# Optimization experiments

Hardware: AMD Instinct MI355X
Metric: run time of the kernel (lower is better)

The kernel has to match this reference:

```python
import jax, jax.numpy as jnp
import numpy as np

N = 100000
E = 1600000
IN_C = 512
HID = 128
OUT_C = 40
NUM_LAYERS = 3
SIGMA = 1.0


def setup_inputs() -> dict:
    key = jax.random.key(0)
    ks = jax.random.split(key, 8)
    x = jax.random.normal(ks[0], (N, IN_C), dtype=jnp.float32)
    edge_index = jax.random.randint(ks[1], (2, E), 0, N, dtype=jnp.int64)
    # input Linear (default torch init scale ~ kaiming uniform; any values fine for a reference)
    W0 = jax.random.normal(ks[2], (HID, IN_C), dtype=jnp.float32) / np.sqrt(IN_C)
    b0 = jnp.zeros((HID,), dtype=jnp.float32)
    # GCNConv weights: normal(0, sigma/sqrt(hidden)) per reset_parameters
    Wc = jax.random.normal(ks[3], (NUM_LAYERS, HID, HID), dtype=jnp.float32) * (SIGMA / np.sqrt(HID))
    bc = jnp.zeros((NUM_LAYERS, HID), dtype=jnp.float32)
    # output Linear
    Wl = jax.random.normal(ks[4], (OUT_C, HID), dtype=jnp.float32) / np.sqrt(HID)
    bl = jnp.zeros((OUT_C,), dtype=jnp.float32)
    return {"x": x, "edge_index": edge_index, "W0": W0, "b0": b0,
            "Wc": Wc, "bc": bc, "Wl": Wl, "bl": bl}


def _gcn_norm(edge_index, num_nodes):
    # PyG GCNConv default: add self-loops, symmetric normalization
    loop = jnp.arange(num_nodes, dtype=edge_index.dtype)
    src = jnp.concatenate([edge_index[0], loop])  # [E + N]
    dst = jnp.concatenate([edge_index[1], loop])
    deg = jax.ops.segment_sum(jnp.ones_like(dst, dtype=jnp.float32), dst,
                              num_segments=num_nodes)
    dinv = jax.lax.rsqrt(deg)  # deg >= 1 thanks to self-loops
    norm = dinv[src] * dinv[dst]  # [E + N]
    return src, dst, norm


def _gcn_conv(h, src, dst, norm, W, b, num_nodes):
    h = h @ W.T                       # [N, HID] transform first (HID small)
    msg = h[src] * norm[:, None]      # gather + scale: [E+N, HID]
    agg = jax.ops.segment_sum(msg, dst, num_segments=num_nodes)
    return agg + b


def reference(x, edge_index, W0, b0, Wc, bc, Wl, bl):
    num_nodes = x.shape[0]
    src, dst, norm = _gcn_norm(edge_index, num_nodes)
    h = jax.nn.relu(x @ W0.T + b0)
    for i in range(Wc.shape[0]):
        h = jax.nn.relu(_gcn_conv(h, src, dst, norm, Wc[i], bc[i], num_nodes))
    logits = h @ Wl.T + bl
    return logits
```

## Files before the change

kernel.cpp:

```cpp
#include <hip/hip_runtime.h>

#define HID 128
#define BSHIFT 10
#define BCAP 20480

typedef _Float16 half8 __attribute__((ext_vector_type(8)));
typedef _Float16 half4v __attribute__((ext_vector_type(4)));
typedef float f32x4 __attribute__((ext_vector_type(4)));


__global__ __launch_bounds__(256) void zero_i32(int* __restrict__ p, int n) {
  int i = blockIdx.x * 256 + threadIdx.x;
  if (i < n) p[i] = 0;
}

__global__ __launch_bounds__(256) void bin_edges(const int* __restrict__ ei,
                                                 int* __restrict__ gcur,
                                                 int2* __restrict__ buf,
                                                 int E, int NB) {
  __shared__ int bcnt[128];
  __shared__ int bbase[128];
  const int tid = threadIdx.x;

  for (int chunk = blockIdx.x * 2048; chunk < E; chunk += gridDim.x * 2048) {
    if (tid < NB) bcnt[tid] = 0;
    __syncthreads();
    int s[8], d[8], slot[8], b[8];
#pragma unroll
    for (int j = 0; j < 8; ++j) {
      int e = chunk + tid + j * 256;
      if (e < E) {
        s[j] = ei[e];
        d[j] = ei[E + e];
        b[j] = d[j] >> BSHIFT;
        slot[j] = atomicAdd(&bcnt[b[j]], 1);
      } else {
        b[j] = -1;
      }
    }
    __syncthreads();
    if (tid < NB && bcnt[tid] > 0) bbase[tid] = atomicAdd(&gcur[tid], bcnt[tid]);
    __syncthreads();
#pragma unroll
    for (int j = 0; j < 8; ++j) {
      if (b[j] >= 0) {
        int pos = bbase[b[j]] + slot[j];
        if (pos < BCAP) buf[(size_t)b[j] * BCAP + pos] = make_int2(s[j], d[j]);
      }
    }
    __syncthreads();
  }
}

__global__ __launch_bounds__(256) void scatter_pad(const int2* __restrict__ buf,
                                                   const int* __restrict__ gcur,
                                                   int* __restrict__ colpad,
                                                   int* __restrict__ cnt,
                                                   float* __restrict__ dinv, int N) {
  __shared__ int lcnt[1 << BSHIFT];
  const int b = blockIdx.x;
  const int base = b << BSHIFT;
  const int tid = threadIdx.x;
  for (int i = tid; i < (1 << BSHIFT); i += 256) lcnt[i] = 0;
  __syncthreads();

  int ne = gcur[b];
  if (ne > BCAP) ne = BCAP;
  const int2* __restrict__ bb = buf + (size_t)b * BCAP;
  for (int i = tid; i < ne; i += 256) {
    int2 p = bb[i];
    int pos = atomicAdd(&lcnt[p.y - base], 1);
    if (pos < 64) colpad[(size_t)p.y * 64 + pos] = p.x;
  }
  __syncthreads();
  for (int i = tid; i < (1 << BSHIFT); i += 256) {
    int n = base + i;
    if (n < N) {
      int c = lcnt[i];
      cnt[n] = c;
      dinv[n] = rsqrtf((float)(c + 1));
    }
  }
}


__global__ __launch_bounds__(256) void cvt_w2(const float* __restrict__ a, int na,
                                              const float* __restrict__ b, int nb,
                                              _Float16* __restrict__ oa,
                                              _Float16* __restrict__ ob) {
  int i = blockIdx.x * 256 + threadIdx.x;
  if (i < na) oa[i] = (_Float16)a[i];
  else if (i < na + nb) ob[i - na] = (_Float16)b[i - na];
}


template <int K, bool CONVA>
__global__ __launch_bounds__(256) void gemm_mfma(const void* __restrict__ Av,
                                                 const _Float16* __restrict__ Wh,
                                                 const float* __restrict__ bias,
                                                 const float* __restrict__ rowscale,
                                                 _Float16* __restrict__ out,
                                                 int N, int do_relu) {
  __shared__ __align__(16) char As[128 * 64 * 2];
  __shared__ __align__(16) char Bs[128 * 64 * 2];

  const int tid = threadIdx.x;
  const int lane = tid & 63;
  const int wave = tid >> 6;
  const int wr = wave >> 1, wc = wave & 1;
  const int row0 = blockIdx.x * 128;

  const float* Af = (const float*)Av;
  const _Float16* Ah = (const _Float16*)Av;

  f32x4 acc[4][4] = {};

  for (int k0 = 0; k0 < K; k0 += 64) {
#pragma unroll
    for (int i = 0; i < 4; ++i) {
      int chunk = tid + i * 256;
      int r = chunk >> 3;
      int q = chunk & 7;
      int gr = row0 + r;
      if (gr >= N) gr = N - 1;
      int byte = (r << 7) | (((q ^ (r & 7)) << 4));
      if (CONVA) {
        const float* src = Af + (size_t)gr * K + k0 + q * 8;
        float4 f0 = *(const float4*)(src);
        float4 f1 = *(const float4*)(src + 4);
        half8 h;
        h[0] = (_Float16)f0.x; h[1] = (_Float16)f0.y;
        h[2] = (_Float16)f0.z; h[3] = (_Float16)f0.w;
        h[4] = (_Float16)f1.x; h[5] = (_Float16)f1.y;
        h[6] = (_Float16)f1.z; h[7] = (_Float16)f1.w;
        *(half8*)(As + byte) = h;
      } else {
        *(half8*)(As + byte) = *(const half8*)(Ah + (size_t)gr * K + k0 + q * 8);
      }
    }
#pragma unroll
    for (int i = 0; i < 4; ++i) {
      int chunk = tid + i * 256;
      int c = chunk >> 3;
      int q = chunk & 7;
      int byte = (c << 7) | (((q ^ (c & 7)) << 4));
      *(half8*)(Bs + byte) = *(const half8*)(Wh + (size_t)c * K + k0 + q * 8);
    }
    __syncthreads();

#pragma unroll
    for (int ks = 0; ks < 2; ++ks) {
      half8 a[4], b[4];
#pragma unroll
      for (int mi = 0; mi < 4; ++mi) {
        int r = wr * 64 + mi * 16 + (lane & 15);
        int q = ks * 4 + (lane >> 4);
        a[mi] = *(const half8*)(As + ((r << 7) | ((q ^ (r & 7)) << 4)));
      }
#pragma unroll
      for (int ni = 0; ni < 4; ++ni) {
        int c = wc * 64 + ni * 16 + (lane & 15);
        int q = ks * 4 + (lane >> 4);
        b[ni] = *(const half8*)(Bs + ((c << 7) | ((q ^ (c & 7)) << 4)));
      }
#pragma unroll
      for (int mi = 0; mi < 4; ++mi)
#pragma unroll
        for (int ni = 0; ni < 4; ++ni)
          acc[mi][ni] = __builtin_amdgcn_mfma_f32_16x16x32_f16(a[mi], b[ni], acc[mi][ni], 0, 0, 0);
    }
    __syncthreads();
  }

  const int cbase = wc * 64 + (lane & 15);
  const int rsub = (lane >> 4) * 4;
#pragma unroll
  for (int mi = 0; mi < 4; ++mi) {
#pragma unroll
    for (int j = 0; j < 4; ++j) {
      int gr = row0 + wr * 64 + mi * 16 + rsub + j;
      if (gr < N) {
        float rs = rowscale ? rowscale[gr] : 1.0f;
#pragma unroll
        for (int ni = 0; ni < 4; ++ni) {
          int c = cbase + ni * 16;
          float v = acc[mi][ni][j] * rs;
          if (bias) v += bias[c];
          if (do_relu) v = fmaxf(v, 0.f);
          out[(size_t)gr * HID + c] = (_Float16)v;
        }
      }
    }
  }
}


__global__ __launch_bounds__(256) void agg_pad(const _Float16* __restrict__ g,
                                               const int* __restrict__ cnt,
                                               const int* __restrict__ colpad,
                                               const float* __restrict__ dinv,
                                               const float* __restrict__ bias,
                                               _Float16* __restrict__ out, int N) {
  int node = blockIdx.x * 4 + (threadIdx.x >> 6);
  if (node >= N) return;
  const int lane = threadIdx.x & 63;
  const int es = lane >> 4;
  const int ch = lane & 15;
  const int deg = cnt[node];
  const int* __restrict__ row = colpad + (size_t)node * 64;

  float acc[8] = {0.f, 0.f, 0.f, 0.f, 0.f, 0.f, 0.f, 0.f};
  int e0 = 0;
  for (; e0 + 16 <= deg; e0 += 16) {
    int i0 = row[e0 + es];
    int i1 = row[e0 + 4 + es];
    int i2 = row[e0 + 8 + es];
    int i3 = row[e0 + 12 + es];
    half8 v0 = *(const half8*)(g + (size_t)i0 * HID + ch * 8);
    half8 v1 = *(const half8*)(g + (size_t)i1 * HID + ch * 8);
    half8 v2 = *(const half8*)(g + (size_t)i2 * HID + ch * 8);
    half8 v3 = *(const half8*)(g + (size_t)i3 * HID + ch * 8);
#pragma unroll
    for (int j = 0; j < 8; ++j)
      acc[j] += ((float)v0[j] + (float)v1[j]) + ((float)v2[j] + (float)v3[j]);
  }
  for (; e0 + 4 <= deg; e0 += 4) {
    int i0 = row[e0 + es];
    half8 v0 = *(const half8*)(g + (size_t)i0 * HID + ch * 8);
#pragma unroll
    for (int j = 0; j < 8; ++j) acc[j] += (float)v0[j];
  }
  const int rem = deg - e0;
  float selfw = 1.0f;
  if (rem > 0) {
    int i0 = (es < rem) ? row[e0 + es] : node;
    half8 v0 = *(const half8*)(g + (size_t)i0 * HID + ch * 8);
#pragma unroll
    for (int j = 0; j < 8; ++j) acc[j] += (float)v0[j];
    selfw = 1.0f - (float)(4 - rem);
  }

#pragma unroll
  for (int j = 0; j < 8; ++j) {
    acc[j] += __shfl_xor(acc[j], 16, 64);
    acc[j] += __shfl_xor(acc[j], 32, 64);
  }

  if (lane < 16) {
    half8 sv = *(const half8*)(g + (size_t)node * HID + ch * 8);
    const float di = dinv[node];
    half8 o;
#pragma unroll
    for (int j = 0; j < 8; ++j) {
      float v = di * (acc[j] + selfw * (float)sv[j]) + bias[ch * 8 + j];
      o[j] = (_Float16)fmaxf(v, 0.f);
    }
    *(half8*)(out + (size_t)node * HID + ch * 8) = o;
  }
}


__global__ __launch_bounds__(256) void gemm40_mfma(const _Float16* __restrict__ h,
                                                   const float* __restrict__ Wl,
                                                   const float* __restrict__ bl,
                                                   float* __restrict__ out, int N) {
  __shared__ __align__(16) _Float16 wlds[48][136];

  const int tid = threadIdx.x;
  const int lane = tid & 63;
  const int wave = tid >> 6;
  const int row0 = blockIdx.x * 128;

#pragma unroll
  for (int i = 0; i < 6; ++i) {
    int idx4 = tid + i * 256;
    int c = idx4 >> 5;
    int ko = (idx4 & 31) * 4;
    float4 v = make_float4(0.f, 0.f, 0.f, 0.f);
    if (c < 40) v = *(const float4*)(Wl + (size_t)c * HID + ko);
    half4v hv;
    hv[0] = (_Float16)v.x; hv[1] = (_Float16)v.y;
    hv[2] = (_Float16)v.z; hv[3] = (_Float16)v.w;
    *(half4v*)&wlds[c][ko] = hv;
  }
  __syncthreads();

  f32x4 acc[2][3] = {};
  const int arow_in = lane & 15;
  const int kq = lane >> 4;

#pragma unroll
  for (int ks = 0; ks < 4; ++ks) {
    half8 a[2], b[3];
#pragma unroll
    for (int mi = 0; mi < 2; ++mi) {
      int gr = row0 + wave * 32 + mi * 16 + arow_in;
      if (gr >= N) gr = N - 1;
      a[mi] = *(const half8*)(h + (size_t)gr * HID + ks * 32 + kq * 8);
    }
#pragma unroll
    for (int ni = 0; ni < 3; ++ni) {
      int c = ni * 16 + arow_in;
      b[ni] = *(const half8*)&wlds[c][ks * 32 + kq * 8];
    }
#pragma unroll
    for (int mi = 0; mi < 2; ++mi)
#pragma unroll
      for (int ni = 0; ni < 3; ++ni)
        acc[mi][ni] = __builtin_amdgcn_mfma_f32_16x16x32_f16(a[mi], b[ni], acc[mi][ni], 0, 0, 0);
  }

  const int rsub = (lane >> 4) * 4;
#pragma unroll
  for (int ni = 0; ni < 3; ++ni) {
    int col = ni * 16 + (lane & 15);
    if (col >= 40) continue;
    float bv = bl[col];
#pragma unroll
    for (int mi = 0; mi < 2; ++mi) {
#pragma unroll
      for (int j = 0; j < 4; ++j) {
        int gr = row0 + wave * 32 + mi * 16 + rsub + j;
        if (gr < N) out[(size_t)gr * 40 + col] = acc[mi][ni][j] + bv;
      }
    }
  }
}


extern "C" void kernel_launch(void* const* d_in, const int* in_sizes, int n_in,
                              void* d_out, int out_size, void* d_ws, size_t ws_size,
                              hipStream_t stream) {
  const float* x = (const float*)d_in[0];
  const int* ei = (const int*)d_in[1];
  const float* W0 = (const float*)d_in[2];
  const float* b0 = (const float*)d_in[3];
  const float* Wc = (const float*)d_in[4];
  const float* bc = (const float*)d_in[5];
  const float* Wl = (const float*)d_in[6];
  const float* bl = (const float*)d_in[7];
  float* out = (float*)d_out;

  const int N = in_sizes[0] / 512;
  const int E = in_sizes[1] / 2;
  const int NB = (N + (1 << BSHIFT) - 1) >> BSHIFT;

  char* ws = (char*)d_ws;
  size_t off = 0;
  auto alloc = [&](size_t bytes) -> char* {
    char* p = ws + off;
    off += (bytes + 511) & ~(size_t)511;
    return p;
  };
  float* dinv = (float*)alloc((size_t)N * 4);
  int* cnt = (int*)alloc((size_t)N * 4);
  int* gcur = (int*)alloc(128 * 4);
  int* colpad = (int*)alloc((size_t)N * 64 * 4);
  int2* bbuf = (int2*)alloc((size_t)NB * BCAP * 8);
  _Float16* hA = (_Float16*)alloc((size_t)N * HID * 2);
  _Float16* hB = (_Float16*)alloc((size_t)N * HID * 2);
  _Float16* hG = (_Float16*)alloc((size_t)N * HID * 2);
  _Float16* W0h = (_Float16*)alloc((size_t)HID * 512 * 2);
  _Float16* Wch = (_Float16*)alloc((size_t)3 * HID * HID * 2);

  const int nb_g = (N + 127) / 128;

  zero_i32<<<1, 256, 0, stream>>>(gcur, 128);
  bin_edges<<<512, 256, 0, stream>>>(ei, gcur, bbuf, E, NB);
  scatter_pad<<<NB, 256, 0, stream>>>(bbuf, gcur, colpad, cnt, dinv, N);

  const int nw0 = HID * 512, nwc = 3 * HID * HID;
  cvt_w2<<<(nw0 + nwc + 255) / 256, 256, 0, stream>>>(W0, nw0, Wc, nwc, W0h, Wch);

  gemm_mfma<512, true><<<nb_g, 256, 0, stream>>>(x, W0h, b0, nullptr, hA, N, 1);

  _Float16* bufs[2] = {hA, hB};
  int cur = 0;
  for (int l = 0; l < 3; ++l) {
    gemm_mfma<128, false><<<nb_g, 256, 0, stream>>>(bufs[cur], Wch + (size_t)l * HID * HID,
                                                    nullptr, dinv, hG, N, 0);
    agg_pad<<<(N + 3) / 4, 256, 0, stream>>>(hG, cnt, colpad, dinv, bc + (size_t)l * HID,
                                             bufs[1 - cur], N);
    cur = 1 - cur;
  }

  gemm40_mfma<<<nb_g, 256, 0, stream>>>(bufs[cur], Wl, bl, out, N);
}
```

Measured before the change: 395.9 us.

## Prefetch next K-tile into registers in GEMM and pre-convert x to fp16

```diff
diff --git a/kernel.cpp b/kernel.cpp
--- a/kernel.cpp
+++ b/kernel.cpp
@@ -93,9 +93,25 @@
   else if (i < na + nb) ob[i - na] = (_Float16)b[i - na];
 }
 
-
-template <int K, bool CONVA>
-__global__ __launch_bounds__(256) void gemm_mfma(const void* __restrict__ Av,
+__global__ __launch_bounds__(256) void cvt_x(const float* __restrict__ in,
+                                             _Float16* __restrict__ out, int n8) {
+  int stride = gridDim.x * 256;
+  for (int i = blockIdx.x * 256 + threadIdx.x; i < n8; i += stride) {
+    const float* src = in + (size_t)i * 8;
+    float4 f0 = *(const float4*)(src);
+    float4 f1 = *(const float4*)(src + 4);
+    half8 h;
+    h[0] = (_Float16)f0.x; h[1] = (_Float16)f0.y;
+    h[2] = (_Float16)f0.z; h[3] = (_Float16)f0.w;
+    h[4] = (_Float16)f1.x; h[5] = (_Float16)f1.y;
+    h[6] = (_Float16)f1.z; h[7] = (_Float16)f1.w;
+    *(half8*)(out + (size_t)i * 8) = h;
+  }
+}
+
+
+template <int K>
+__global__ __launch_bounds__(256) void gemm_mfma(const _Float16* __restrict__ Ah,
                                                  const _Float16* __restrict__ Wh,
                                                  const float* __restrict__ bias,
                                                  const float* __restrict__ rowscale,
@@ -110,41 +126,42 @@
   const int wr = wave >> 1, wc = wave & 1;
   const int row0 = blockIdx.x * 128;
 
-  const float* Af = (const float*)Av;
-  const _Float16* Ah = (const _Float16*)Av;
+  int stbyte[4];
+  const _Float16* asrc[4];
+  const _Float16* bsrc[4];
+#pragma unroll
+  for (int i = 0; i < 4; ++i) {
+    int chunk = tid + i * 256;
+    int r = chunk >> 3, q = chunk & 7;
+    int gr = row0 + r;
+    if (gr >= N) gr = N - 1;
+    stbyte[i] = (r << 7) | ((q ^ (r & 7)) << 4);
+    asrc[i] = Ah + (size_t)gr * K + q * 8;
+    bsrc[i] = Wh + (size_t)r * K + q * 8;
+  }
+
+  half8 ga[4], gb[4];
+#pragma unroll
+  for (int i = 0; i < 4; ++i) {
+    ga[i] = *(const half8*)(asrc[i]);
+    gb[i] = *(const half8*)(bsrc[i]);
+  }
 
   f32x4 acc[4][4] = {};
 
   for (int k0 = 0; k0 < K; k0 += 64) {
+    __syncthreads();
 #pragma unroll
     for (int i = 0; i < 4; ++i) {
-      int chunk = tid + i * 256;
-      int r = chunk >> 3;
-      int q = chunk & 7;
-      int gr = row0 + r;
-      if (gr >= N) gr = N - 1;
-      int byte = (r << 7) | (((q ^ (r & 7)) << 4));
-      if (CONVA) {
-        const float* src = Af + (size_t)gr * K + k0 + q * 8;
-        float4 f0 = *(const float4*)(src);
-        float4 f1 = *(const float4*)(src + 4);
-        half8 h;
-        h[0] = (_Float16)f0.x; h[1] = (_Float16)f0.y;
-        h[2] = (_Float16)f0.z; h[3] = (_Float16)f0.w;
-        h[4] = (_Float16)f1.x; h[5] = (_Float16)f1.y;
-        h[6] = (_Float16)f1.z; h[7] = (_Float16)f1.w;
-        *(half8*)(As + byte) = h;
-      } else {
-        *(half8*)(As + byte) = *(const half8*)(Ah + (size_t)gr * K + k0 + q * 8);
-      }
-    }
-#pragma unroll
-    for (int i = 0; i < 4; ++i) {
-      int chunk = tid + i * 256;
-      int c = chunk >> 3;
-      int q = chunk & 7;
-      int byte = (c << 7) | (((q ^ (c & 7)) << 4));
-      *(half8*)(Bs + byte) = *(const half8*)(Wh + (size_t)c * K + k0 + q * 8);
+      *(half8*)(As + stbyte[i]) = ga[i];
+      *(half8*)(Bs + stbyte[i]) = gb[i];
+    }
+    if (k0 + 64 < K) {
+#pragma unroll
+      for (int i = 0; i < 4; ++i) {
+        ga[i] = *(const half8*)(asrc[i] + k0 + 64);
+        gb[i] = *(const half8*)(bsrc[i] + k0 + 64);
+      }
     }
     __syncthreads();
 
@@ -169,7 +186,6 @@
         for (int ni = 0; ni < 4; ++ni)
           acc[mi][ni] = __builtin_amdgcn_mfma_f32_16x16x32_f16(a[mi], b[ni], acc[mi][ni], 0, 0, 0);
     }
-    __syncthreads();
   }
 
   const int cbase = wc * 64 + (lane & 15);
@@ -357,6 +373,7 @@
   int* gcur = (int*)alloc(128 * 4);
   int* colpad = (int*)alloc((size_t)N * 64 * 4);
   int2* bbuf = (int2*)alloc((size_t)NB * BCAP * 8);
+  _Float16* xh = (_Float16*)alloc((size_t)N * 512 * 2);
   _Float16* hA = (_Float16*)alloc((size_t)N * HID * 2);
   _Float16* hB = (_Float16*)alloc((size_t)N * HID * 2);
   _Float16* hG = (_Float16*)alloc((size_t)N * HID * 2);
@@ -371,14 +388,15 @@
 
   const int nw0 = HID * 512, nwc = 3 * HID * HID;
   cvt_w2<<<(nw0 + nwc + 255) / 256, 256, 0, stream>>>(W0, nw0, Wc, nwc, W0h, Wch);
-
-  gemm_mfma<512, true><<<nb_g, 256, 0, stream>>>(x, W0h, b0, nullptr, hA, N, 1);
+  cvt_x<<<2048, 256, 0, stream>>>(x, xh, N * 64);
+
+  gemm_mfma<512><<<nb_g, 256, 0, stream>>>(xh, W0h, b0, nullptr, hA, N, 1);
 
   _Float16* bufs[2] = {hA, hB};
   int cur = 0;
   for (int l = 0; l < 3; ++l) {
-    gemm_mfma<128, false><<<nb_g, 256, 0, stream>>>(bufs[cur], Wch + (size_t)l * HID * HID,
-                                                    nullptr, dinv, hG, N, 0);
+    gemm_mfma<128><<<nb_g, 256, 0, stream>>>(bufs[cur], Wch + (size_t)l * HID * HID,
+                                             nullptr, dinv, hG, N, 0);
     agg_pad<<<(N + 3) / 4, 256, 0, stream>>>(hG, cnt, colpad, dinv, bc + (size_t)l * HID,
                                              bufs[1 - cur], N);
     cur = 1 - cur;
```

After: 429.0 us. 8.4% more time.

## Replace LDS-staged GEMM with direct-from-global MFMA operand loads

Applied to the files above, without the earlier changes.

```diff
diff --git a/kernel.cpp b/kernel.cpp
--- a/kernel.cpp
+++ b/kernel.cpp
@@ -95,99 +95,77 @@
 
 
 template <int K, bool CONVA>
-__global__ __launch_bounds__(256) void gemm_mfma(const void* __restrict__ Av,
-                                                 const _Float16* __restrict__ Wh,
-                                                 const float* __restrict__ bias,
-                                                 const float* __restrict__ rowscale,
-                                                 _Float16* __restrict__ out,
-                                                 int N, int do_relu) {
-  __shared__ __align__(16) char As[128 * 64 * 2];
-  __shared__ __align__(16) char Bs[128 * 64 * 2];
-
+__global__ __launch_bounds__(256) void gemm_direct(const void* __restrict__ Av,
+                                                   const _Float16* __restrict__ Wh,
+                                                   const float* __restrict__ bias,
+                                                   const float* __restrict__ rowscale,
+                                                   _Float16* __restrict__ out,
+                                                   int N, int do_relu) {
   const int tid = threadIdx.x;
   const int lane = tid & 63;
   const int wave = tid >> 6;
-  const int wr = wave >> 1, wc = wave & 1;
   const int row0 = blockIdx.x * 128;
 
   const float* Af = (const float*)Av;
   const _Float16* Ah = (const _Float16*)Av;
 
-  f32x4 acc[4][4] = {};
-
-  for (int k0 = 0; k0 < K; k0 += 64) {
-#pragma unroll
-    for (int i = 0; i < 4; ++i) {
-      int chunk = tid + i * 256;
-      int r = chunk >> 3;
-      int q = chunk & 7;
-      int gr = row0 + r;
-      if (gr >= N) gr = N - 1;
-      int byte = (r << 7) | (((q ^ (r & 7)) << 4));
-      if (CONVA) {
-        const float* src = Af + (size_t)gr * K + k0 + q * 8;
-        float4 f0 = *(const float4*)(src);
-        float4 f1 = *(const float4*)(src + 4);
+  const int rsel = lane & 15;
+  const int q = lane >> 4;
+
+  int gr[2];
+#pragma unroll
+  for (int mi = 0; mi < 2; ++mi) {
+    int r = row0 + wave * 32 + mi * 16 + rsel;
+    gr[mi] = (r < N) ? r : (N - 1);
+  }
+
+  f32x4 acc[2][8] = {};
+
+#pragma unroll 2
+  for (int ks = 0; ks < K / 32; ++ks) {
+    half8 a[2];
+#pragma unroll
+    for (int mi = 0; mi < 2; ++mi) {
+      if constexpr (CONVA) {
+        const float* src = Af + (size_t)gr[mi] * K + ks * 32 + q * 8;
+        f32x4 f0 = *(const f32x4*)(src);
+        f32x4 f1 = *(const f32x4*)(src + 4);
         half8 h;
-        h[0] = (_Float16)f0.x; h[1] = (_Float16)f0.y;
-        h[2] = (_Float16)f0.z; h[3] = (_Float16)f0.w;
-        h[4] = (_Float16)f1.x; h[5] = (_Float16)f1.y;
-        h[6] = (_Float16)f1.z; h[7] = (_Float16)f1.w;
-        *(half8*)(As + byte) = h;
+        h[0] = (_Float16)f0[0]; h[1] = (_Float16)f0[1];
+        h[2] = (_Float16)f0[2]; h[3] = (_Float16)f0[3];
+        h[4] = (_Float16)f1[0]; h[5] = (_Float16)f1[1];
+        h[6] = (_Float16)f1[2]; h[7] = (_Float16)f1[3];
+        a[mi] = h;
       } else {
-        *(half8*)(As + byte) = *(const half8*)(Ah + (size_t)gr * K + k0 + q * 8);
-      }
-    }
-#pragma unroll
-    for (int i = 0; i < 4; ++i) {
-      int chunk = tid + i * 256;
-      int c = chunk >> 3;
-      int q = chunk & 7;
-      int byte = (c << 7) | (((q ^ (c & 7)) << 4));
-      *(half8*)(Bs + byte) = *(const half8*)(Wh + (size_t)c * K + k0 + q * 8);
-    }
-    __syncthreads();
-
-#pragma unroll
-    for (int ks = 0; ks < 2; ++ks) {
-      half8 a[4], b[4];
-#pragma unroll
-      for (int mi = 0; mi < 4; ++mi) {
-        int r = wr * 64 + mi * 16 + (lane & 15);
-        int q = ks * 4 + (lane >> 4);
-        a[mi] = *(const half8*)(As + ((r << 7) | ((q ^ (r & 7)) << 4)));
-      }
-#pragma unroll
-      for (int ni = 0; ni < 4; ++ni) {
-        int c = wc * 64 + ni * 16 + (lane & 15);
-        int q = ks * 4 + (lane >> 4);
-        b[ni] = *(const half8*)(Bs + ((c << 7) | ((q ^ (c & 7)) << 4)));
-      }
-#pragma unroll
-      for (int mi = 0; mi < 4; ++mi)
-#pragma unroll
-        for (int ni = 0; ni < 4; ++ni)
-          acc[mi][ni] = __builtin_amdgcn_mfma_f32_16x16x32_f16(a[mi], b[ni], acc[mi][ni], 0, 0, 0);
-    }
-    __syncthreads();
-  }
-
-  const int cbase = wc * 64 + (lane & 15);
+        a[mi] = *(const half8*)(Ah + (size_t)gr[mi] * K + ks * 32 + q * 8);
+      }
+    }
+    half8 b[8];
+#pragma unroll
+    for (int ni = 0; ni < 8; ++ni)
+      b[ni] = *(const half8*)(Wh + (size_t)(ni * 16 + rsel) * K + ks * 32 + q * 8);
+#pragma unroll
+    for (int mi = 0; mi < 2; ++mi)
+#pragma unroll
+      for (int ni = 0; ni < 8; ++ni)
+        acc[mi][ni] = __builtin_amdgcn_mfma_f32_16x16x32_f16(a[mi], b[ni], acc[mi][ni], 0, 0, 0);
+  }
+
   const int rsub = (lane >> 4) * 4;
 #pragma unroll
-  for (int mi = 0; mi < 4; ++mi) {
+  for (int mi = 0; mi < 2; ++mi) {
 #pragma unroll
     for (int j = 0; j < 4; ++j) {
-      int gr = row0 + wr * 64 + mi * 16 + rsub + j;
-      if (gr < N) {
-        float rs = rowscale ? rowscale[gr] : 1.0f;
-#pragma unroll
-        for (int ni = 0; ni < 4; ++ni) {
-          int c = cbase + ni * 16;
+      int grow = row0 + wave * 32 + mi * 16 + rsub + j;
+      if (grow < N) {
+        float rs = rowscale ? rowscale[grow] : 1.0f;
+#pragma unroll
+        for (int ni = 0; ni < 8; ++ni) {
+          int c = ni * 16 + rsel;
           float v = acc[mi][ni][j] * rs;
           if (bias) v += bias[c];
           if (do_relu) v = fmaxf(v, 0.f);
-          out[(size_t)gr * HID + c] = (_Float16)v;
+          out[(size_t)grow * HID + c] = (_Float16)v;
         }
       }
     }
@@ -372,13 +350,13 @@
   const int nw0 = HID * 512, nwc = 3 * HID * HID;
   cvt_w2<<<(nw0 + nwc + 255) / 256, 256, 0, stream>>>(W0, nw0, Wc, nwc, W0h, Wch);
 
-  gemm_mfma<512, true><<<nb_g, 256, 0, stream>>>(x, W0h, b0, nullptr, hA, N, 1);
+  gemm_direct<512, true><<<nb_g, 256, 0, stream>>>(x, W0h, b0, nullptr, hA, N, 1);
 
   _Float16* bufs[2] = {hA, hB};
   int cur = 0;
   for (int l = 0; l < 3; ++l) {
-    gemm_mfma<128, false><<<nb_g, 256, 0, stream>>>(bufs[cur], Wch + (size_t)l * HID * HID,
-                                                    nullptr, dinv, hG, N, 0);
+    gemm_direct<128, false><<<nb_g, 256, 0, stream>>>(bufs[cur], Wch + (size_t)l * HID * HID,
+                                                      nullptr, dinv, hG, N, 0);
     agg_pad<<<(N + 3) / 4, 256, 0, stream>>>(hG, cnt, colpad, dinv, bc + (size_t)l * HID,
                                              bufs[1 - cur], N);
     cur = 1 - cur;
```

Result: slower. 464.0 us (+17.2%).
